# Kernel optimization log

Measured on AMD Instinct MI355X. Metric: run time of the kernel, lower is better.

## Reference

```python
import jax, jax.numpy as jnp
import numpy as np

B, S, DM, H, NSYN = 4, 2048, 768, 12, 4
HD = DM // H  # 64
EPS = 1e-12
SCALE = float(DM / H) ** -0.5  # 1/sqrt(head_dim)


def setup_inputs() -> dict:
    key = jax.random.key(0)
    ks = jax.random.split(key, 16)
    p = 0.02
    return {
        "hidden_states": jax.random.normal(ks[0], (B, S, DM), jnp.float32),
        "attention_mask": jnp.zeros((B, 1, 1, S), jnp.float32),
        "addi_key": jax.random.normal(ks[1], (B, NSYN, S, HD), jnp.float32),
        "addi_value": jax.random.normal(ks[2], (B, NSYN, S, HD), jnp.float32),
        "Wq": jax.random.normal(ks[3], (DM, DM), jnp.float32) * p,
        "bq": jnp.zeros((DM,), jnp.float32),
        "Wk": jax.random.normal(ks[4], (DM, DM), jnp.float32) * p,
        "bk": jnp.zeros((DM,), jnp.float32),
        "Wv": jax.random.normal(ks[5], (DM, DM), jnp.float32) * p,
        "bv": jnp.zeros((DM,), jnp.float32),
        "Wo": jax.random.normal(ks[6], (DM, DM), jnp.float32) * p,
        "bo": jnp.zeros((DM,), jnp.float32),
        "ln_g": jnp.ones((DM,), jnp.float32),
        "ln_b": jnp.zeros((DM,), jnp.float32),
    }


def _heads(x):
    # [B,S,DM] -> [B,H,S,HD]
    return x.reshape(B, S, H, HD).transpose(0, 2, 1, 3)


def reference(hidden_states, attention_mask, addi_key, addi_value,
              Wq, bq, Wk, bk, Wv, bv, Wo, bo, ln_g, ln_b):
    x = hidden_states
    q = _heads(jnp.einsum('bsi,oi->bso', x, Wq) + bq)
    k = _heads(jnp.einsum('bsi,oi->bso', x, Wk) + bk)
    v = _heads(jnp.einsum('bsi,oi->bso', x, Wv) + bv)
    # additive key/value injection on first NSYN heads
    k = k.at[:, :NSYN].add(addi_key)
    v = v.at[:, :NSYN].add(addi_value)
    scores = jnp.einsum('bhqd,bhkd->bhqk', q, k) * SCALE + attention_mask
    probs = jax.nn.softmax(scores, axis=-1)
    ctx = jnp.einsum('bhqk,bhkd->bhqd', probs, v)
    ctx = ctx.transpose(0, 2, 1, 3).reshape(B, S, DM)
    out = jnp.einsum('bsi,oi->bso', ctx, Wo) + bo
    h = out + x  # residual
    mu = jnp.mean(h, axis=-1, keepdims=True)
    var = jnp.mean((h - mu) ** 2, axis=-1, keepdims=True)
    return (h - mu) * jax.lax.rsqrt(var + EPS) * ln_g + ln_b
```

## Files before the change

### kernel.cpp

```cpp
#include <hip/hip_runtime.h>


typedef __bf16 bf16;
typedef __bf16 bf16x8 __attribute__((ext_vector_type(8)));
typedef __bf16 bf16x4 __attribute__((ext_vector_type(4)));
typedef float floatx4 __attribute__((ext_vector_type(4)));

#define BB 4
#define SS 2048
#define DM 768
#define HH 12
#define HD 64
#define NSYN 4
#define MM (BB*SS)
#define KK DM
#define SCALE 0.125f
#define LOG2E 1.4426950408889634f

#define N_X   ((size_t)MM * DM)
#define N_W   ((size_t)DM * DM)
#define N_M   ((size_t)BB * SS)

#if __has_builtin(__builtin_amdgcn_exp2f)
#define EXP2(x) __builtin_amdgcn_exp2f(x)
#else
#define EXP2(x) exp2f(x)
#endif

#define ASYNC16(gp, lp)                                                        \
    __builtin_amdgcn_global_load_lds(                                          \
        (const __attribute__((address_space(1))) unsigned int*)(gp),           \
        (__attribute__((address_space(3))) unsigned int*)(lp), 16, 0, 0)

__global__ __launch_bounds__(256) void cvt_kernel(
    const float* __restrict__ x,
    const float* __restrict__ Wq, const float* __restrict__ Wk,
    const float* __restrict__ Wv, const float* __restrict__ Wo,
    const float* __restrict__ mask,
    bf16* __restrict__ xb,
    bf16* __restrict__ Wqb, bf16* __restrict__ Wkb,
    bf16* __restrict__ Wvb, bf16* __restrict__ Wob,
    float* __restrict__ ml2e)
{
    const size_t nx4 = N_X / 4, nw4 = N_W / 4, nm4 = N_M / 4;
    size_t i = (size_t)blockIdx.x * blockDim.x + threadIdx.x;
    if (i >= nx4 + 4 * nw4) {
        size_t off = i - nx4 - 4 * nw4;
        if (off < nm4) {
            float4 m = *(const float4*)(mask + off * 4);
            float4 o = { m.x * LOG2E, m.y * LOG2E, m.z * LOG2E, m.w * LOG2E };
            *(float4*)(ml2e + off * 4) = o;
        }
        return;
    }
    const float* src; bf16* dst; size_t off;
    if (i < nx4)                { src = x;  dst = xb;  off = i; }
    else if (i < nx4 + nw4)     { src = Wq; dst = Wqb; off = i - nx4; }
    else if (i < nx4 + 2*nw4)   { src = Wk; dst = Wkb; off = i - nx4 - nw4; }
    else if (i < nx4 + 3*nw4)   { src = Wv; dst = Wvb; off = i - nx4 - 2*nw4; }
    else                        { src = Wo; dst = Wob; off = i - nx4 - 3*nw4; }
    float4 v = *(const float4*)(src + off * 4);
    bf16x4 o = { (bf16)v.x, (bf16)v.y, (bf16)v.z, (bf16)v.w };
    *(bf16x4*)(dst + off * 4) = o;
}

template<int ORD>
__device__ __forceinline__ void gemm_mainloop(
    const bf16* __restrict__ A, const bf16* __restrict__ Bw,
    int tileM, int tileN, bf16* As, bf16* Bs, floatx4 acc[4][4])
{
    const int tid  = threadIdx.x;
    const int lane = tid & 63;
    const int wave = tid >> 6;
    const int wm = wave >> 1, wn = wave & 1;
    const int l15 = lane & 15, quad = lane >> 4;

    const int r0  = wave * 32 + (lane >> 2);
    const int cl  = (lane & 3) ^ (r0 & 3);
    const bf16* gA = A  + (size_t)(tileM * 128 + r0) * KK + cl * 8;
    const bf16* gB = Bw + (size_t)(tileN * 128 + r0) * KK + cl * 8;
    bf16* lA = As + (wave * 32) * 32;
    bf16* lB = Bs + (wave * 32) * 32;

    ASYNC16(gA,           lA);
    ASYNC16(gA + 16 * KK, lA + 16 * 32);
    ASYNC16(gB,           lB);
    ASYNC16(gB + 16 * KK, lB + 16 * 32);
    __syncthreads();

    const int fpc = quad ^ (l15 & 3);
    for (int kt = 0; kt < KK / 32; ++kt) {
        const int cur = kt & 1;
        if (kt + 1 < KK / 32) {
            const int nb = (1 - cur) * 4096;
            ASYNC16(gA + (kt + 1) * 32,           lA + nb);
            ASYNC16(gA + (kt + 1) * 32 + 16 * KK, lA + nb + 16 * 32);
            ASYNC16(gB + (kt + 1) * 32,           lB + nb);
            ASYNC16(gB + (kt + 1) * 32 + 16 * KK, lB + nb + 16 * 32);
        }
        const bf16* cA = As + cur * 4096;
        const bf16* cB = Bs + cur * 4096;
        bf16x8 af[4], bfr[4];
        #pragma unroll
        for (int i = 0; i < 4; ++i)
            af[i] = *(const bf16x8*)(cA + (wm * 64 + i * 16 + l15) * 32 + fpc * 8);
        #pragma unroll
        for (int j = 0; j < 4; ++j)
            bfr[j] = *(const bf16x8*)(cB + (wn * 64 + j * 16 + l15) * 32 + fpc * 8);
        #pragma unroll
        for (int i = 0; i < 4; ++i)
            #pragma unroll
            for (int j = 0; j < 4; ++j)
                acc[i][j] = (ORD == 0)
                    ? __builtin_amdgcn_mfma_f32_16x16x32_bf16(af[i], bfr[j], acc[i][j], 0, 0, 0)
                    : __builtin_amdgcn_mfma_f32_16x16x32_bf16(bfr[j], af[i], acc[i][j], 0, 0, 0);
        __syncthreads();
    }
}

__global__ __launch_bounds__(256) void qkv_kernel(
    const bf16* __restrict__ xb,
    const bf16* __restrict__ Wqb, const float* __restrict__ bq,
    const bf16* __restrict__ Wkb, const float* __restrict__ bk,
    const bf16* __restrict__ Wvb, const float* __restrict__ bv,
    const float* __restrict__ addi_key, const float* __restrict__ addi_value,
    bf16* __restrict__ qbuf, bf16* __restrict__ kbuf, bf16* __restrict__ vtbuf)
{
    __shared__ __align__(16) bf16 As[2 * 128 * 32];
    __shared__ __align__(16) bf16 Bs[2 * 128 * 32];
    const int u = blockIdx.x;
    const int tileM = u & 63;
    const int r     = u >> 6;
    const int tileN = r % 6;
    const int z     = r / 6;
    const bf16* W     = (z == 0) ? Wqb : (z == 1) ? Wkb : Wvb;
    const float* bias = (z == 0) ? bq  : (z == 1) ? bk  : bv;

    floatx4 acc[4][4];
    #pragma unroll
    for (int i = 0; i < 4; ++i)
        #pragma unroll
        for (int j = 0; j < 4; ++j) { floatx4 zv = {0.f, 0.f, 0.f, 0.f}; acc[i][j] = zv; }

    const int lane = threadIdx.x & 63, wave = threadIdx.x >> 6;
    const int wm = wave >> 1, wn = wave & 1, l15 = lane & 15, quad = lane >> 4;

    if (z == 2) {
        gemm_mainloop<0>(xb, W, tileM, tileN, As, Bs, acc);
        #pragma unroll
        for (int i = 0; i < 4; ++i) {
            #pragma unroll
            for (int j = 0; j < 4; ++j) {
                const int o = tileN * 128 + wn * 64 + j * 16 + l15;
                const float bv_ = bias[o];
                const int h = o >> 6, d = o & 63;
                const int sg0 = tileM * 128 + wm * 64 + i * 16 + quad * 4;
                const int b = sg0 >> 11, s0 = sg0 & 2047;
                float vv[4];
                #pragma unroll
                for (int rr = 0; rr < 4; ++rr) {
                    vv[rr] = acc[i][j][rr] + bv_;
                    if (h < NSYN)
                        vv[rr] += addi_value[(((size_t)b * NSYN + h) * SS + s0 + rr) * HD + d];
                }
                bf16x4 pk = { (bf16)vv[0], (bf16)vv[1], (bf16)vv[2], (bf16)vv[3] };
                *(bf16x4*)(vtbuf + (((size_t)b * HH + h) * HD + d) * SS + s0) = pk;
            }
        }
    } else {
        gemm_mainloop<1>(xb, W, tileM, tileN, As, Bs, acc);
        #pragma unroll
        for (int i = 0; i < 4; ++i) {
            const int sg = tileM * 128 + wm * 64 + i * 16 + l15;
            const int b = sg >> 11, s = sg & 2047;
            #pragma unroll
            for (int j = 0; j < 4; ++j) {
                const int o0 = tileN * 128 + wn * 64 + j * 16 + quad * 4;
                const int h = o0 >> 6, d0 = o0 & 63;
                float4 b4 = *(const float4*)(bias + o0);
                float vv[4] = { acc[i][j][0] + b4.x, acc[i][j][1] + b4.y,
                                acc[i][j][2] + b4.z, acc[i][j][3] + b4.w };
                if (z == 1 && h < NSYN) {
                    float4 a4 = *(const float4*)(addi_key +
                        (((size_t)b * NSYN + h) * SS + s) * HD + d0);
                    vv[0] += a4.x; vv[1] += a4.y; vv[2] += a4.z; vv[3] += a4.w;
                }
                if (z == 0) {
                    bf16x4 pk = { (bf16)(vv[0] * SCALE), (bf16)(vv[1] * SCALE),
                                  (bf16)(vv[2] * SCALE), (bf16)(vv[3] * SCALE) };
                    *(bf16x4*)(qbuf + (((size_t)b * HH + h) * SS + s) * HD + d0) = pk;
                } else {
                    bf16x4 pk = { (bf16)vv[0], (bf16)vv[1], (bf16)vv[2], (bf16)vv[3] };
                    *(bf16x4*)(kbuf + (((size_t)b * HH + h) * SS + s) * HD + d0) = pk;
                }
            }
        }
    }
}

__global__ __launch_bounds__(256, 4) void attn_kernel(
    const bf16* __restrict__ qbuf, const bf16* __restrict__ kbuf,
    const bf16* __restrict__ vtbuf, const float* __restrict__ ml2e,
    bf16* __restrict__ ctx)
{
    __shared__ __align__(16) bf16 Ks[64 * 64];
    __shared__ __align__(16) bf16 Vt[64 * 64];
    __shared__ __align__(16) bf16 Ps[4][32 * 72];

    const int u  = blockIdx.x;
    const int bh = u % 48;
    const int qt = u / 48;
    const int b  = bh / 12;
    const int h  = bh % 12;
    const size_t bhs = ((size_t)b * HH + h) * SS * HD;
    const int tid = threadIdx.x, lane = tid & 63, wave = tid >> 6;
    const int l15 = lane & 15, quad = lane >> 4;
    const int q0 = qt * 128 + wave * 32;

    const int sr  = wave * 16 + (lane >> 3);
    const int scl = (lane & 7) ^ (sr & 7);
    const bf16* gK = kbuf  + bhs + (size_t)sr * HD + scl * 8;
    const bf16* gV = vtbuf + bhs + (size_t)sr * SS + scl * 8;
    bf16* lK = Ks + (wave * 16) * 64;
    bf16* lV = Vt + (wave * 16) * 64;

    bf16x8 qf[2][2];
    #pragma unroll
    for (int n = 0; n < 2; ++n)
        #pragma unroll
        for (int c = 0; c < 2; ++c)
            qf[n][c] = *(const bf16x8*)(qbuf + bhs +
                (size_t)(q0 + n * 16 + l15) * HD + c * 32 + quad * 8);

    floatx4 acco[2][4];
    #pragma unroll
    for (int n = 0; n < 2; ++n)
        #pragma unroll
        for (int t = 0; t < 4; ++t) { floatx4 zv = {0.f, 0.f, 0.f, 0.f}; acco[n][t] = zv; }
    float lrun[2] = { 0.f, 0.f };

    const float* mb = ml2e + (size_t)b * SS;
    bf16* Pw = Ps[wave];

    for (int kt = 0; kt < SS / 64; ++kt) {
        __syncthreads();
        ASYNC16(gK + (size_t)kt * 64 * HD,            lK);
        ASYNC16(gK + (size_t)kt * 64 * HD + 8 * HD,   lK + 8 * 64);
        ASYNC16(gV + kt * 64,                         lV);
        ASYNC16(gV + kt * 64 + 8 * SS,                lV + 8 * 64);
        __syncthreads();

        floatx4 sacc[2][4];
        #pragma unroll
        for (int n = 0; n < 2; ++n)
            #pragma unroll
            for (int j = 0; j < 4; ++j) { floatx4 zv = {0.f, 0.f, 0.f, 0.f}; sacc[n][j] = zv; }
        #pragma unroll
        for (int c = 0; c < 2; ++c) {
            const int pc = (4 * c + quad) ^ (l15 & 7);
            #pragma unroll
            for (int j = 0; j < 4; ++j) {
                bf16x8 af = *(const bf16x8*)(Ks + (j * 16 + l15) * 64 + pc * 8);
                #pragma unroll
                for (int n = 0; n < 2; ++n)
                    sacc[n][j] = __builtin_amdgcn_mfma_f32_16x16x32_bf16(af, qf[n][c], sacc[n][j], 0, 0, 0);
            }
        }

        float rs[2] = { 0.f, 0.f };
        #pragma unroll
        for (int j = 0; j < 4; ++j) {
            float4 mk = *(const float4*)(mb + kt * 64 + j * 16 + quad * 4);
            #pragma unroll
            for (int n = 0; n < 2; ++n) {
                float p0 = EXP2(__builtin_fmaf(sacc[n][j][0], LOG2E, mk.x));
                float p1 = EXP2(__builtin_fmaf(sacc[n][j][1], LOG2E, mk.y));
                float p2 = EXP2(__builtin_fmaf(sacc[n][j][2], LOG2E, mk.z));
                float p3 = EXP2(__builtin_fmaf(sacc[n][j][3], LOG2E, mk.w));
                rs[n] += (p0 + p1) + (p2 + p3);
                bf16x4 pk = { (bf16)p0, (bf16)p1, (bf16)p2, (bf16)p3 };
                *(bf16x4*)(Pw + (n * 16 + l15) * 72 + j * 16 + quad * 4) = pk;
            }
        }
        #pragma unroll
        for (int n = 0; n < 2; ++n) {
            float rr = rs[n];
            rr += __shfl_xor(rr, 16);
            rr += __shfl_xor(rr, 32);
            lrun[n] += rr;
        }

        #pragma unroll
        for (int c = 0; c < 2; ++c) {
            const int pc = (4 * c + quad) ^ (l15 & 7);
            bf16x8 pfr[2];
            #pragma unroll
            for (int n = 0; n < 2; ++n)
                pfr[n] = *(const bf16x8*)(Pw + (n * 16 + l15) * 72 + c * 32 + quad * 8);
            #pragma unroll
            for (int t = 0; t < 4; ++t) {
                bf16x8 af = *(const bf16x8*)(Vt + (t * 16 + l15) * 64 + pc * 8);
                #pragma unroll
                for (int n = 0; n < 2; ++n)
                    acco[n][t] = __builtin_amdgcn_mfma_f32_16x16x32_bf16(af, pfr[n], acco[n][t], 0, 0, 0);
            }
        }
    }

    #pragma unroll
    for (int n = 0; n < 2; ++n) {
        const float inv = 1.0f / lrun[n];
        bf16* crow = ctx + ((size_t)(b * SS + q0 + n * 16 + l15)) * DM + h * HD;
        #pragma unroll
        for (int t = 0; t < 4; ++t) {
            bf16x4 ov = { (bf16)(acco[n][t][0] * inv), (bf16)(acco[n][t][1] * inv),
                          (bf16)(acco[n][t][2] * inv), (bf16)(acco[n][t][3] * inv) };
            *(bf16x4*)(crow + t * 16 + quad * 4) = ov;
        }
    }
}

__global__ __launch_bounds__(256) void oproj_kernel(
    const bf16* __restrict__ ctx, const bf16* __restrict__ Wob,
    const float* __restrict__ bo, const float* __restrict__ x,
    bf16* __restrict__ hbuf)
{
    __shared__ __align__(16) bf16 As[2 * 128 * 32];
    __shared__ __align__(16) bf16 Bs[2 * 128 * 32];
    const int u = blockIdx.x;
    const int tileM = u & 63;
    const int tileN = u >> 6;

    floatx4 acc[4][4];
    #pragma unroll
    for (int i = 0; i < 4; ++i)
        #pragma unroll
        for (int j = 0; j < 4; ++j) { floatx4 zv = {0.f, 0.f, 0.f, 0.f}; acc[i][j] = zv; }

    gemm_mainloop<1>(ctx, Wob, tileM, tileN, As, Bs, acc);

    const int lane = threadIdx.x & 63, wave = threadIdx.x >> 6;
    const int wm = wave >> 1, wn = wave & 1, l15 = lane & 15, quad = lane >> 4;
    #pragma unroll
    for (int i = 0; i < 4; ++i) {
        const int sg = tileM * 128 + wm * 64 + i * 16 + l15;
        #pragma unroll
        for (int j = 0; j < 4; ++j) {
            const int o0 = tileN * 128 + wn * 64 + j * 16 + quad * 4;
            float4 b4 = *(const float4*)(bo + o0);
            float4 r4 = *(const float4*)(x + (size_t)sg * DM + o0);
            bf16x4 pk = { (bf16)(acc[i][j][0] + b4.x + r4.x),
                          (bf16)(acc[i][j][1] + b4.y + r4.y),
                          (bf16)(acc[i][j][2] + b4.z + r4.z),
                          (bf16)(acc[i][j][3] + b4.w + r4.w) };
            *(bf16x4*)(hbuf + (size_t)sg * DM + o0) = pk;
        }
    }
}

__global__ __launch_bounds__(256) void ln_kernel(
    const bf16* __restrict__ hbuf, const float* __restrict__ g,
    const float* __restrict__ be, float* __restrict__ out)
{
    const int row  = blockIdx.x * 4 + (threadIdx.x >> 6);
    const int lane = threadIdx.x & 63;
    const bf16* hr = hbuf + (size_t)row * DM;

    bf16x8 va = *(const bf16x8*)(hr + lane * 8);
    bf16x4 vb = *(const bf16x4*)(hr + 512 + lane * 4);
    float v[12];
    #pragma unroll
    for (int i = 0; i < 8; ++i) v[i] = (float)va[i];
    #pragma unroll
    for (int i = 0; i < 4; ++i) v[8 + i] = (float)vb[i];

    float s = 0.f;
    #pragma unroll
    for (int i = 0; i < 12; ++i) s += v[i];
    #pragma unroll
    for (int m = 1; m < 64; m <<= 1) s += __shfl_xor(s, m);
    const float mu = s * (1.0f / DM);

    float s2 = 0.f;
    #pragma unroll
    for (int i = 0; i < 12; ++i) { v[i] -= mu; s2 += v[i] * v[i]; }
    #pragma unroll
    for (int m = 1; m < 64; m <<= 1) s2 += __shfl_xor(s2, m);
    const float rsv = rsqrtf(s2 * (1.0f / DM) + 1e-12f);

    float* orow = out + (size_t)row * DM;
    const int c0 = lane * 8, c1 = 512 + lane * 4;
    float4 g0 = *(const float4*)(g + c0),     g1 = *(const float4*)(g + c0 + 4);
    float4 g2 = *(const float4*)(g + c1);
    float4 b0 = *(const float4*)(be + c0),    b1 = *(const float4*)(be + c0 + 4);
    float4 b2 = *(const float4*)(be + c1);
    float4 o0 = { v[0]*rsv*g0.x + b0.x, v[1]*rsv*g0.y + b0.y,
                  v[2]*rsv*g0.z + b0.z, v[3]*rsv*g0.w + b0.w };
    float4 o1 = { v[4]*rsv*g1.x + b1.x, v[5]*rsv*g1.y + b1.y,
                  v[6]*rsv*g1.z + b1.z, v[7]*rsv*g1.w + b1.w };
    float4 o2 = { v[8]*rsv*g2.x + b2.x, v[9]*rsv*g2.y + b2.y,
                  v[10]*rsv*g2.z + b2.z, v[11]*rsv*g2.w + b2.w };
    *(float4*)(orow + c0)     = o0;
    *(float4*)(orow + c0 + 4) = o1;
    *(float4*)(orow + c1)     = o2;
}

extern "C" void kernel_launch(void* const* d_in, const int* in_sizes, int n_in,
                              void* d_out, int out_size, void* d_ws, size_t ws_size,
                              hipStream_t stream)
{
    const float* x    = (const float*)d_in[0];
    const float* mask = (const float*)d_in[1];
    const float* akey = (const float*)d_in[2];
    const float* aval = (const float*)d_in[3];
    const float* Wq = (const float*)d_in[4];  const float* bq = (const float*)d_in[5];
    const float* Wk = (const float*)d_in[6];  const float* bk = (const float*)d_in[7];
    const float* Wv = (const float*)d_in[8];  const float* bv = (const float*)d_in[9];
    const float* Wo = (const float*)d_in[10]; const float* bo = (const float*)d_in[11];
    const float* lng = (const float*)d_in[12]; const float* lnb = (const float*)d_in[13];
    float* outp = (float*)d_out;

    const size_t nqkv = (size_t)BB * HH * SS * HD;
    char* ws = (char*)d_ws;
    bf16*  xb   = (bf16*)ws;   ws += N_X  * sizeof(bf16);
    bf16*  Wqb  = (bf16*)ws;   ws += N_W  * sizeof(bf16);
    bf16*  Wkb  = (bf16*)ws;   ws += N_W  * sizeof(bf16);
    bf16*  Wvb  = (bf16*)ws;   ws += N_W  * sizeof(bf16);
    bf16*  Wob  = (bf16*)ws;   ws += N_W  * sizeof(bf16);
    float* ml2e = (float*)ws;  ws += N_M  * sizeof(float);
    bf16*  qbuf = (bf16*)ws;   ws += nqkv * sizeof(bf16);
    bf16*  kbuf = (bf16*)ws;   ws += nqkv * sizeof(bf16);
    bf16*  vtbuf= (bf16*)ws;   ws += nqkv * sizeof(bf16);
    bf16*  ctxb = (bf16*)ws;   ws += nqkv * sizeof(bf16);
    bf16*  hbuf = (bf16*)ws;   ws += nqkv * sizeof(bf16);

    const size_t ncvt = (N_X + 4 * N_W + N_M) / 4;
    const int cvt_blocks = (int)((ncvt + 255) / 256);
    cvt_kernel<<<cvt_blocks, 256, 0, stream>>>(x, Wq, Wk, Wv, Wo, mask,
                                               xb, Wqb, Wkb, Wvb, Wob, ml2e);

    qkv_kernel<<<1152, 256, 0, stream>>>(xb, Wqb, bq, Wkb, bk, Wvb, bv, akey, aval,
                                         qbuf, kbuf, vtbuf);
    attn_kernel<<<768, 256, 0, stream>>>(qbuf, kbuf, vtbuf, ml2e, ctxb);
    oproj_kernel<<<384, 256, 0, stream>>>(ctxb, Wob, bo, x, hbuf);
    ln_kernel<<<MM / 4, 256, 0, stream>>>(hbuf, lng, lnb, outp);
}
```

Before: 299.6 us.

## Shrink GEMM N-tiles to 64 and attention blocks to two waves for more blocks

```diff
diff --git a/kernel.cpp b/kernel.cpp
--- a/kernel.cpp
+++ b/kernel.cpp
@@ -65,50 +65,49 @@
 }
 
 template<int ORD>
-__device__ __forceinline__ void gemm_mainloop(
+__device__ __forceinline__ void gemm_mainloop64(
     const bf16* __restrict__ A, const bf16* __restrict__ Bw,
-    int tileM, int tileN, bf16* As, bf16* Bs, floatx4 acc[4][4])
+    int tileM, int tileN, bf16* As, bf16* Bs, floatx4 acc[2][4])
 {
     const int tid  = threadIdx.x;
     const int lane = tid & 63;
     const int wave = tid >> 6;
-    const int wm = wave >> 1, wn = wave & 1;
     const int l15 = lane & 15, quad = lane >> 4;
 
-    const int r0  = wave * 32 + (lane >> 2);
-    const int cl  = (lane & 3) ^ (r0 & 3);
-    const bf16* gA = A  + (size_t)(tileM * 128 + r0) * KK + cl * 8;
-    const bf16* gB = Bw + (size_t)(tileN * 128 + r0) * KK + cl * 8;
+    const int r0a = wave * 32 + (lane >> 2);
+    const int r0b = wave * 16 + (lane >> 2);
+    const int cl  = (lane & 3) ^ ((lane >> 2) & 3);
+    const bf16* gA = A  + (size_t)(tileM * 128 + r0a) * KK + cl * 8;
+    const bf16* gB = Bw + (size_t)(tileN *  64 + r0b) * KK + cl * 8;
     bf16* lA = As + (wave * 32) * 32;
-    bf16* lB = Bs + (wave * 32) * 32;
+    bf16* lB = Bs + (wave * 16) * 32;
 
     ASYNC16(gA,           lA);
     ASYNC16(gA + 16 * KK, lA + 16 * 32);
     ASYNC16(gB,           lB);
-    ASYNC16(gB + 16 * KK, lB + 16 * 32);
     __syncthreads();
 
     const int fpc = quad ^ (l15 & 3);
     for (int kt = 0; kt < KK / 32; ++kt) {
         const int cur = kt & 1;
         if (kt + 1 < KK / 32) {
-            const int nb = (1 - cur) * 4096;
-            ASYNC16(gA + (kt + 1) * 32,           lA + nb);
-            ASYNC16(gA + (kt + 1) * 32 + 16 * KK, lA + nb + 16 * 32);
-            ASYNC16(gB + (kt + 1) * 32,           lB + nb);
-            ASYNC16(gB + (kt + 1) * 32 + 16 * KK, lB + nb + 16 * 32);
+            const int nbA = (1 - cur) * 4096;
+            const int nbB = (1 - cur) * 2048;
+            ASYNC16(gA + (kt + 1) * 32,           lA + nbA);
+            ASYNC16(gA + (kt + 1) * 32 + 16 * KK, lA + nbA + 16 * 32);
+            ASYNC16(gB + (kt + 1) * 32,           lB + nbB);
         }
         const bf16* cA = As + cur * 4096;
-        const bf16* cB = Bs + cur * 4096;
-        bf16x8 af[4], bfr[4];
-        #pragma unroll
-        for (int i = 0; i < 4; ++i)
-            af[i] = *(const bf16x8*)(cA + (wm * 64 + i * 16 + l15) * 32 + fpc * 8);
+        const bf16* cB = Bs + cur * 2048;
+        bf16x8 af[2], bfr[4];
+        #pragma unroll
+        for (int i = 0; i < 2; ++i)
+            af[i] = *(const bf16x8*)(cA + (wave * 32 + i * 16 + l15) * 32 + fpc * 8);
         #pragma unroll
         for (int j = 0; j < 4; ++j)
-            bfr[j] = *(const bf16x8*)(cB + (wn * 64 + j * 16 + l15) * 32 + fpc * 8);
-        #pragma unroll
-        for (int i = 0; i < 4; ++i)
+            bfr[j] = *(const bf16x8*)(cB + (j * 16 + l15) * 32 + fpc * 8);
+        #pragma unroll
+        for (int i = 0; i < 2; ++i)
             #pragma unroll
             for (int j = 0; j < 4; ++j)
                 acc[i][j] = (ORD == 0)
@@ -127,35 +126,35 @@
     bf16* __restrict__ qbuf, bf16* __restrict__ kbuf, bf16* __restrict__ vtbuf)
 {
     __shared__ __align__(16) bf16 As[2 * 128 * 32];
-    __shared__ __align__(16) bf16 Bs[2 * 128 * 32];
+    __shared__ __align__(16) bf16 Bs[2 * 64 * 32];
     const int u = blockIdx.x;
     const int tileM = u & 63;
     const int r     = u >> 6;
-    const int tileN = r % 6;
-    const int z     = r / 6;
+    const int tileN = r % 12;
+    const int z     = r / 12;
     const bf16* W     = (z == 0) ? Wqb : (z == 1) ? Wkb : Wvb;
     const float* bias = (z == 0) ? bq  : (z == 1) ? bk  : bv;
 
-    floatx4 acc[4][4];
-    #pragma unroll
-    for (int i = 0; i < 4; ++i)
+    floatx4 acc[2][4];
+    #pragma unroll
+    for (int i = 0; i < 2; ++i)
         #pragma unroll
         for (int j = 0; j < 4; ++j) { floatx4 zv = {0.f, 0.f, 0.f, 0.f}; acc[i][j] = zv; }
 
     const int lane = threadIdx.x & 63, wave = threadIdx.x >> 6;
-    const int wm = wave >> 1, wn = wave & 1, l15 = lane & 15, quad = lane >> 4;
+    const int l15 = lane & 15, quad = lane >> 4;
 
     if (z == 2) {
-        gemm_mainloop<0>(xb, W, tileM, tileN, As, Bs, acc);
-        #pragma unroll
-        for (int i = 0; i < 4; ++i) {
+        gemm_mainloop64<0>(xb, W, tileM, tileN, As, Bs, acc);
+        #pragma unroll
+        for (int i = 0; i < 2; ++i) {
+            const int sg0 = tileM * 128 + wave * 32 + i * 16 + quad * 4;
+            const int b = sg0 >> 11, s0 = sg0 & 2047;
             #pragma unroll
             for (int j = 0; j < 4; ++j) {
-                const int o = tileN * 128 + wn * 64 + j * 16 + l15;
+                const int o = tileN * 64 + j * 16 + l15;
                 const float bv_ = bias[o];
                 const int h = o >> 6, d = o & 63;
-                const int sg0 = tileM * 128 + wm * 64 + i * 16 + quad * 4;
-                const int b = sg0 >> 11, s0 = sg0 & 2047;
                 float vv[4];
                 #pragma unroll
                 for (int rr = 0; rr < 4; ++rr) {
@@ -168,14 +167,14 @@
             }
         }
     } else {
-        gemm_mainloop<1>(xb, W, tileM, tileN, As, Bs, acc);
-        #pragma unroll
-        for (int i = 0; i < 4; ++i) {
-            const int sg = tileM * 128 + wm * 64 + i * 16 + l15;
+        gemm_mainloop64<1>(xb, W, tileM, tileN, As, Bs, acc);
+        #pragma unroll
+        for (int i = 0; i < 2; ++i) {
+            const int sg = tileM * 128 + wave * 32 + i * 16 + l15;
             const int b = sg >> 11, s = sg & 2047;
             #pragma unroll
             for (int j = 0; j < 4; ++j) {
-                const int o0 = tileN * 128 + wn * 64 + j * 16 + quad * 4;
+                const int o0 = tileN * 64 + j * 16 + quad * 4;
                 const int h = o0 >> 6, d0 = o0 & 63;
                 float4 b4 = *(const float4*)(bias + o0);
                 float vv[4] = { acc[i][j][0] + b4.x, acc[i][j][1] + b4.y,
@@ -198,14 +197,14 @@
     }
 }
 
-__global__ __launch_bounds__(256, 4) void attn_kernel(
+__global__ __launch_bounds__(128, 3) void attn_kernel(
     const bf16* __restrict__ qbuf, const bf16* __restrict__ kbuf,
     const bf16* __restrict__ vtbuf, const float* __restrict__ ml2e,
     bf16* __restrict__ ctx)
 {
     __shared__ __align__(16) bf16 Ks[64 * 64];
     __shared__ __align__(16) bf16 Vt[64 * 64];
-    __shared__ __align__(16) bf16 Ps[4][32 * 72];
+    __shared__ __align__(16) bf16 Ps[2][32 * 72];
 
     const int u  = blockIdx.x;
     const int bh = u % 48;
@@ -215,14 +214,14 @@
     const size_t bhs = ((size_t)b * HH + h) * SS * HD;
     const int tid = threadIdx.x, lane = tid & 63, wave = tid >> 6;
     const int l15 = lane & 15, quad = lane >> 4;
-    const int q0 = qt * 128 + wave * 32;
-
-    const int sr  = wave * 16 + (lane >> 3);
-    const int scl = (lane & 7) ^ (sr & 7);
+    const int q0 = qt * 64 + wave * 32;
+
+    const int sr  = wave * 32 + (lane >> 3);
+    const int scl = (lane & 7) ^ ((lane >> 3) & 7);
     const bf16* gK = kbuf  + bhs + (size_t)sr * HD + scl * 8;
     const bf16* gV = vtbuf + bhs + (size_t)sr * SS + scl * 8;
-    bf16* lK = Ks + (wave * 16) * 64;
-    bf16* lV = Vt + (wave * 16) * 64;
+    bf16* lK = Ks + (wave * 32) * 64;
+    bf16* lV = Vt + (wave * 32) * 64;
 
     bf16x8 qf[2][2];
     #pragma unroll
@@ -244,10 +243,11 @@
 
     for (int kt = 0; kt < SS / 64; ++kt) {
         __syncthreads();
-        ASYNC16(gK + (size_t)kt * 64 * HD,            lK);
-        ASYNC16(gK + (size_t)kt * 64 * HD + 8 * HD,   lK + 8 * 64);
-        ASYNC16(gV + kt * 64,                         lV);
-        ASYNC16(gV + kt * 64 + 8 * SS,                lV + 8 * 64);
+        #pragma unroll
+        for (int p = 0; p < 4; ++p) {
+            ASYNC16(gK + ((size_t)kt * 64 + p * 8) * HD, lK + p * 512);
+            ASYNC16(gV + (size_t)p * 8 * SS + kt * 64,   lV + p * 512);
+        }
         __syncthreads();
 
         floatx4 sacc[2][4];
@@ -267,7 +267,6 @@
             }
         }
 
-        float rs[2] = { 0.f, 0.f };
         #pragma unroll
         for (int j = 0; j < 4; ++j) {
             float4 mk = *(const float4*)(mb + kt * 64 + j * 16 + quad * 4);
@@ -277,17 +276,10 @@
                 float p1 = EXP2(__builtin_fmaf(sacc[n][j][1], LOG2E, mk.y));
                 float p2 = EXP2(__builtin_fmaf(sacc[n][j][2], LOG2E, mk.z));
                 float p3 = EXP2(__builtin_fmaf(sacc[n][j][3], LOG2E, mk.w));
-                rs[n] += (p0 + p1) + (p2 + p3);
+                lrun[n] += (p0 + p1) + (p2 + p3);
                 bf16x4 pk = { (bf16)p0, (bf16)p1, (bf16)p2, (bf16)p3 };
                 *(bf16x4*)(Pw + (n * 16 + l15) * 72 + j * 16 + quad * 4) = pk;
             }
-        }
-        #pragma unroll
-        for (int n = 0; n < 2; ++n) {
-            float rr = rs[n];
-            rr += __shfl_xor(rr, 16);
-            rr += __shfl_xor(rr, 32);
-            lrun[n] += rr;
         }
 
         #pragma unroll
@@ -309,6 +301,12 @@
 
     #pragma unroll
     for (int n = 0; n < 2; ++n) {
+        lrun[n] += __shfl_xor(lrun[n], 16);
+        lrun[n] += __shfl_xor(lrun[n], 32);
+    }
+
+    #pragma unroll
+    for (int n = 0; n < 2; ++n) {
         const float inv = 1.0f / lrun[n];
         bf16* crow = ctx + ((size_t)(b * SS + q0 + n * 16 + l15)) * DM + h * HD;
         #pragma unroll
@@ -326,27 +324,27 @@
     bf16* __restrict__ hbuf)
 {
     __shared__ __align__(16) bf16 As[2 * 128 * 32];
-    __shared__ __align__(16) bf16 Bs[2 * 128 * 32];
+    __shared__ __align__(16) bf16 Bs[2 * 64 * 32];
     const int u = blockIdx.x;
     const int tileM = u & 63;
     const int tileN = u >> 6;
 
-    floatx4 acc[4][4];
-    #pragma unroll
-    for (int i = 0; i < 4; ++i)
+    floatx4 acc[2][4];
+    #pragma unroll
+    for (int i = 0; i < 2; ++i)
         #pragma unroll
         for (int j = 0; j < 4; ++j) { floatx4 zv = {0.f, 0.f, 0.f, 0.f}; acc[i][j] = zv; }
 
-    gemm_mainloop<1>(ctx, Wob, tileM, tileN, As, Bs, acc);
+    gemm_mainloop64<1>(ctx, Wob, tileM, tileN, As, Bs, acc);
 
     const int lane = threadIdx.x & 63, wave = threadIdx.x >> 6;
-    const int wm = wave >> 1, wn = wave & 1, l15 = lane & 15, quad = lane >> 4;
-    #pragma unroll
-    for (int i = 0; i < 4; ++i) {
-        const int sg = tileM * 128 + wm * 64 + i * 16 + l15;
+    const int l15 = lane & 15, quad = lane >> 4;
+    #pragma unroll
+    for (int i = 0; i < 2; ++i) {
+        const int sg = tileM * 128 + wave * 32 + i * 16 + l15;
         #pragma unroll
         for (int j = 0; j < 4; ++j) {
-            const int o0 = tileN * 128 + wn * 64 + j * 16 + quad * 4;
+            const int o0 = tileN * 64 + j * 16 + quad * 4;
             float4 b4 = *(const float4*)(bo + o0);
             float4 r4 = *(const float4*)(x + (size_t)sg * DM + o0);
             bf16x4 pk = { (bf16)(acc[i][j][0] + b4.x + r4.x),
@@ -439,9 +437,9 @@
     cvt_kernel<<<cvt_blocks, 256, 0, stream>>>(x, Wq, Wk, Wv, Wo, mask,
                                                xb, Wqb, Wkb, Wvb, Wob, ml2e);
 
-    qkv_kernel<<<1152, 256, 0, stream>>>(xb, Wqb, bq, Wkb, bk, Wvb, bv, akey, aval,
+    qkv_kernel<<<2304, 256, 0, stream>>>(xb, Wqb, bq, Wkb, bk, Wvb, bv, akey, aval,
                                          qbuf, kbuf, vtbuf);
-    attn_kernel<<<768, 256, 0, stream>>>(qbuf, kbuf, vtbuf, ml2e, ctxb);
-    oproj_kernel<<<384, 256, 0, stream>>>(ctxb, Wob, bo, x, hbuf);
+    attn_kernel<<<1536, 128, 0, stream>>>(qbuf, kbuf, vtbuf, ml2e, ctxb);
+    oproj_kernel<<<768, 256, 0, stream>>>(ctxb, Wob, bo, x, hbuf);
     ln_kernel<<<MM / 4, 256, 0, stream>>>(hbuf, lng, lnb, outp);
 }
```

After: 282.4 us. 5.7% less time.
